# Kernel optimization log

Measured on AMD Instinct MI355X. Metric: run time of the kernel, lower is better.

Reference implementation:

```python
import jax, jax.numpy as jnp
import numpy as np

B, SEQ, D, H, C = 256, 512, 256, 1024, 10
S = SEQ - 1  # module uses seq_length - 1 timesteps


def _kaiming(key, shape):
    fan_in = shape[0]
    return jax.random.normal(key, shape, dtype=jnp.float32) * np.float32(np.sqrt(2.0 / fan_in))


def setup_inputs() -> dict:
    key = jax.random.key(0)
    ks = jax.random.split(key, 12)
    inp = {
        "x": jax.random.randint(ks[0], (B, SEQ), 0, SEQ),
        "emb": jax.random.normal(ks[1], (SEQ, D), dtype=jnp.float32),
        # forward-direction LSTM cell (only modulation g and input i gates affect output
        # because of the source bug: f_out = o_out = sigmoid(i_input))
        "Wgx_f": _kaiming(ks[2], (D, H)), "Wgh_f": _kaiming(ks[3], (H, H)), "bg_f": jnp.zeros((H,), jnp.float32),
        "Wix_f": _kaiming(ks[4], (D, H)), "Wih_f": _kaiming(ks[5], (H, H)), "bi_f": jnp.zeros((H,), jnp.float32),
        # backward-direction LSTM cell
        "Wgx_b": _kaiming(ks[6], (D, H)), "Wgh_b": _kaiming(ks[7], (H, H)), "bg_b": jnp.zeros((H,), jnp.float32),
        "Wix_b": _kaiming(ks[8], (D, H)), "Wih_b": _kaiming(ks[9], (H, H)), "bi_b": jnp.zeros((H,), jnp.float32),
        # prediction head
        "Wp": _kaiming(ks[10], (2 * H, C)), "bp": jnp.zeros((C,), jnp.float32),
    }
    return inp


def _run_lstm(xs, Wgx, Wgh, bg, Wix, Wih, bi):
    # xs: [S, B, D]; returns final hidden state [B, H]
    def step(carry, xt):
        h, c = carry
        g = jnp.tanh(xt @ Wgx + h @ Wgh + bg)
        i = jax.nn.sigmoid(xt @ Wix + h @ Wih + bi)
        # source bug: forget and output gates both equal the input gate i
        c = g * i + i * c
        h = jnp.tanh(c) * i
        return (h, c), None
    h0 = jnp.zeros((xs.shape[1], Wgh.shape[0]), xs.dtype)
    (h, _), _ = jax.lax.scan(step, (h0, h0), xs)
    return h


def reference(x, emb, Wgx_f, Wgh_f, bg_f, Wix_f, Wih_f, bi_f,
              Wgx_b, Wgh_b, bg_b, Wix_b, Wih_b, bi_b, Wp, bp):
    e = emb[x]                              # [B, SEQ, D]
    xs = jnp.transpose(e[:, :S], (1, 0, 2))  # [S, B, D]; last token unused (seq_length-1 steps)
    hf = _run_lstm(xs, Wgx_f, Wgh_f, bg_f, Wix_f, Wih_f, bi_f)
    hb = _run_lstm(xs[::-1], Wgx_b, Wgh_b, bg_b, Wix_b, Wih_b, bi_b)
    Hcat = jnp.concatenate([hf, hb], axis=1)  # [B, 2H]
    return Hcat @ Wp + bp                     # [B, C]
```

## Files before the change

kernel.cpp:

```cpp
#include <hip/hip_runtime.h>
#include <hip/hip_fp16.h>

typedef _Float16 half8 __attribute__((ext_vector_type(8)));
typedef float f32x4 __attribute__((ext_vector_type(4)));
typedef unsigned u32x4 __attribute__((ext_vector_type(4)));
typedef unsigned long long u64;

#define B_ 256
#define SEQ_ 512
#define D_ 256
#define H_ 1024
#define C_ 10
#define S_ 511
#define KB_ 40
#define NPK_ 2048
#define NTF_ 128
#define LP_ 84

#define WPK_HALVES (2*KB_*NTF_*512)
#define EMBH_OFF   (WPK_HALVES*2)
#define EMBH_HALVES (SEQ_*D_)
#define HPK_OFF    (EMBH_OFF + EMBH_HALVES*2)
#define HPK_PER_PAR (2*32*16*64*8)
#define HFIN_OFF   (HPK_OFF + 2*HPK_PER_PAR*2)
#define HFIN_FLOATS (2*B_*H_)
#define BIAS_OFF   (HFIN_OFF + HFIN_FLOATS*4)
#define BAR_OFF    (BIAS_OFF + 2*NPK_*4)
#define BAR_WORDS  (8*32*16)
#define XT_OFF     (BAR_OFF + BAR_WORDS*4)
#define XT_INTS    (SEQ_*B_)
#define XCD_OFF    (XT_OFF + XT_INTS*4)
#define XCD_WORDS  256

__device__ __forceinline__ float fast_sigm(float x) {
    return __builtin_amdgcn_rcpf(1.f + __builtin_amdgcn_exp2f(-1.442695041f * x));
}
__device__ __forceinline__ float fast_tanh(float x) {
    return 1.f - 2.f * __builtin_amdgcn_rcpf(1.f + __builtin_amdgcn_exp2f(2.885390082f * x));
}
__device__ __forceinline__ half8 load_h_uc(const _Float16* p) {
    u64 two[2];
    two[0] = __hip_atomic_load((const u64*)p,     __ATOMIC_RELAXED, __HIP_MEMORY_SCOPE_SYSTEM);
    two[1] = __hip_atomic_load((const u64*)p + 1, __ATOMIC_RELAXED, __HIP_MEMORY_SCOPE_SYSTEM);
    half8 r; __builtin_memcpy(&r, two, 16); return r;
}

__global__ void convert_kernel(
    const int* __restrict__ x, const float* __restrict__ emb,
    const float* __restrict__ Wgx_f, const float* __restrict__ Wgh_f, const float* __restrict__ bg_f,
    const float* __restrict__ Wix_f, const float* __restrict__ Wih_f, const float* __restrict__ bi_f,
    const float* __restrict__ Wgx_b, const float* __restrict__ Wgh_b, const float* __restrict__ bg_b,
    const float* __restrict__ Wix_b, const float* __restrict__ Wih_b, const float* __restrict__ bi_b,
    _Float16* __restrict__ Wpk, _Float16* __restrict__ embh, float* __restrict__ biaspk,
    unsigned* __restrict__ bar, int* __restrict__ xT, unsigned* __restrict__ xcdid)
{
    int idx = blockIdx.x * 256 + threadIdx.x;
    if (idx < WPK_HALVES) {
        int j = idx & 7;
        int L = (idx >> 3) & 63;
        int rest = idx >> 9;
        int ntf = rest & (NTF_ - 1);
        int rest2 = rest >> 7;
        int kb = rest2 % KB_;
        int d  = rest2 / KB_;
        int k = kb*32 + ((L >> 4) << 3) + j;
        int p = (ntf << 4) + (L & 15);
        int gate = (p >> 5) & 1;
        int u = ((p >> 6) << 5) + (p & 31);
        float v;
        if (k < D_) {
            const float* W = d ? (gate ? Wix_b : Wgx_b) : (gate ? Wix_f : Wgx_f);
            v = W[k*H_ + u];
        } else {
            const float* W = d ? (gate ? Wih_b : Wgh_b) : (gate ? Wih_f : Wgh_f);
            v = W[(k - D_)*H_ + u];
        }
        Wpk[idx] = (_Float16)v;
    } else if (idx < WPK_HALVES + EMBH_HALVES) {
        int i2 = idx - WPK_HALVES;
        embh[i2] = (_Float16)emb[i2];
    } else if (idx < WPK_HALVES + EMBH_HALVES + 2*NPK_) {
        int i3 = idx - (WPK_HALVES + EMBH_HALVES);
        int d = i3 >> 11;
        int p = i3 & (NPK_ - 1);
        int gate = (p >> 5) & 1;
        int u = ((p >> 6) << 5) + (p & 31);
        const float* bsrc = d ? (gate ? bi_b : bg_b) : (gate ? bi_f : bg_f);
        biaspk[i3] = bsrc[u];
    } else if (idx < WPK_HALVES + EMBH_HALVES + 2*NPK_ + BAR_WORDS) {
        bar[idx - (WPK_HALVES + EMBH_HALVES + 2*NPK_)] = 0u;
    } else if (idx < WPK_HALVES + EMBH_HALVES + 2*NPK_ + BAR_WORDS + XT_INTS) {
        int i5 = idx - (WPK_HALVES + EMBH_HALVES + 2*NPK_ + BAR_WORDS);
        int t = i5 >> 8;
        int m = i5 & (B_ - 1);
        xT[i5] = x[m*SEQ_ + t];
    } else if (idx < WPK_HALVES + EMBH_HALVES + 2*NPK_ + BAR_WORDS + XT_INTS + XCD_WORDS) {
        xcdid[idx - (WPK_HALVES + EMBH_HALVES + 2*NPK_ + BAR_WORDS + XT_INTS)] = 0u;
    }
}

#define ISSUE_PAIR(buf, pr)                                                                     \
    { _Pragma("unroll")                                                                         \
      for (int j2 = 0; j2 < 2; ++j2) {                                                          \
        _Pragma("unroll")                                                                       \
        for (int mt = 0; mt < 4; ++mt) {                                                        \
            const _Float16* hp = hrd + (size_t)(((8*w + (pr)*2 + j2)*16 + (mtblk*4 + mt))*64 + lane)*8; \
            asm volatile("global_load_dwordx4 %0, %1, off sc0" : "=v"(buf[j2*4+mt]) : "v"(hp)); \
        } } }

#define MFMA_PAIR(buf, pr)                                                                      \
    { _Pragma("unroll")                                                                         \
      for (int j2 = 0; j2 < 2; ++j2)                                                            \
        _Pragma("unroll")                                                                       \
        for (int mt = 0; mt < 4; ++mt)                                                          \
          _Pragma("unroll")                                                                     \
          for (int nt = 0; nt < 4; ++nt)                                                        \
            acc[mt][nt] = __builtin_amdgcn_mfma_f32_16x16x32_f16(buf[j2*4+mt], wfh[(pr)*2+j2][nt], acc[mt][nt], 0, 0, 0); }

__global__ __launch_bounds__(256, 1) void persistent_kernel(
    const int* __restrict__ xT, const _Float16* __restrict__ embh,
    const _Float16* __restrict__ Wpk, const float* __restrict__ biaspk,
    _Float16* __restrict__ hpk, float* __restrict__ hfinal,
    unsigned* __restrict__ bar, unsigned* __restrict__ xcdid)
{
    __shared__ float lds[4][64][LP_];

    int group = blockIdx.x & 7;
    int dir   = group >> 2;
    int mtblk = group & 3;
    int ntb   = blockIdx.x >> 3;
    int w    = threadIdx.x >> 6;
    int lane = threadIdx.x & 63;
    int q    = lane >> 4;
    int c16  = lane & 15;
    int u0   = q * 8;

    unsigned* gflags = bar + group * (32*16);

    unsigned myxcc;
    asm volatile("s_getreg_b32 %0, hwreg(HW_REG_XCC_ID)" : "=s"(myxcc));
    myxcc &= 15u;
    if (threadIdx.x == 0)
        __hip_atomic_store(&xcdid[blockIdx.x], myxcc | 0x100u, __ATOMIC_RELAXED, __HIP_MEMORY_SCOPE_SYSTEM);

    const _Float16* Wd = Wpk + (size_t)dir * (KB_*NTF_*512);

    half8 wfx[2][4], wfh[8][4];
    #pragma unroll
    for (int kx = 0; kx < 2; ++kx) {
        #pragma unroll
        for (int nt = 0; nt < 4; ++nt)
            wfx[kx][nt] = *(const half8*)(Wd + (((size_t)(2*w + kx)*NTF_ + (ntb*4 + nt))*64 + lane)*8);
    }
    #pragma unroll
    for (int i = 0; i < 8; ++i) {
        #pragma unroll
        for (int nt = 0; nt < 4; ++nt)
            wfh[i][nt] = *(const half8*)(Wd + (((size_t)(8 + 8*w + i)*NTF_ + (ntb*4 + nt))*64 + lane)*8);
    }

    float bgr[8], bir[8];
    #pragma unroll
    for (int j = 0; j < 8; ++j) {
        bgr[j] = biaspk[dir*NPK_ + ntb*64 + u0 + j];
        bir[j] = biaspk[dir*NPK_ + ntb*64 + 32 + u0 + j];
    }

    bool fast;
    {
        unsigned idv = myxcc | 0x100u;
        for (;;) {
            if (lane < 32)
                idv = __hip_atomic_load(&xcdid[lane*8 + group], __ATOMIC_RELAXED, __HIP_MEMORY_SCOPE_SYSTEM);
            if (__all(idv >= 0x100u)) break;
            __builtin_amdgcn_s_sleep(1);
        }
        fast = __all(idv == (myxcc | 0x100u));
    }

    float creg[8];
    #pragma unroll
    for (int j = 0; j < 8; ++j) creg[j] = 0.f;

    #pragma unroll 1
    for (int t = 0; t < S_; ++t) {
        const _Float16* hrd = hpk + (size_t)(t & 1) * HPK_PER_PAR + dir*(32*16*64*8);
        _Float16*       hwr = hpk + (size_t)((t & 1) ^ 1) * HPK_PER_PAR + dir*(32*16*64*8);
        int t_eff = dir ? (S_ - 1 - t) : t;

        int xr[4];
        #pragma unroll
        for (int mt = 0; mt < 4; ++mt)
            xr[mt] = xT[t_eff*B_ + mtblk*64 + mt*16 + c16];

        f32x4 acc[4][4];
        #pragma unroll
        for (int a = 0; a < 4; ++a)
            #pragma unroll
            for (int b = 0; b < 4; ++b) {
                acc[a][b][0] = 0.f; acc[a][b][1] = 0.f; acc[a][b][2] = 0.f; acc[a][b][3] = 0.f;
            }

        #pragma unroll
        for (int kx = 0; kx < 2; ++kx) {
            int kb = 2*w + kx;
            half8 a[4];
            #pragma unroll
            for (int mt = 0; mt < 4; ++mt)
                a[mt] = *(const half8*)(embh + xr[mt]*D_ + kb*32 + q*8);
            #pragma unroll
            for (int mt = 0; mt < 4; ++mt) {
                #pragma unroll
                for (int nt = 0; nt < 4; ++nt)
                    acc[mt][nt] = __builtin_amdgcn_mfma_f32_16x16x32_f16(a[mt], wfx[kx][nt], acc[mt][nt], 0, 0, 0);
            }
        }

        if (t > 0) {
            unsigned gen = (unsigned)t;
            if (fast) {
                u32x4 fv = {gen, gen, gen, gen};
                for (;;) {
                    if (lane < 32) {
                        const unsigned* fp = gflags + lane*16;
                        asm volatile("global_load_dwordx4 %0, %1, off sc0\n\ts_waitcnt vmcnt(0)"
                                     : "=v"(fv) : "v"(fp) : "memory");
                    }
                    if (__all(fv[0] >= gen && fv[1] >= gen && fv[2] >= gen && fv[3] >= gen)) break;
                    __builtin_amdgcn_s_sleep(1);
                }
                half8 aE[8], aO[8];
                ISSUE_PAIR(aE, 0);
                ISSUE_PAIR(aO, 1);
                asm volatile("s_waitcnt vmcnt(8)" ::: "memory");
                __builtin_amdgcn_sched_barrier(0);
                MFMA_PAIR(aE, 0);
                ISSUE_PAIR(aE, 2);
                asm volatile("s_waitcnt vmcnt(8)" ::: "memory");
                __builtin_amdgcn_sched_barrier(0);
                MFMA_PAIR(aO, 1);
                ISSUE_PAIR(aO, 3);
                asm volatile("s_waitcnt vmcnt(8)" ::: "memory");
                __builtin_amdgcn_sched_barrier(0);
                MFMA_PAIR(aE, 2);
                asm volatile("s_waitcnt vmcnt(0)" ::: "memory");
                __builtin_amdgcn_sched_barrier(0);
                MFMA_PAIR(aO, 3);
            } else {
                unsigned v = gen;
                for (;;) {
                    if (lane < 32)
                        v = __hip_atomic_load(&gflags[lane*16], __ATOMIC_RELAXED, __HIP_MEMORY_SCOPE_SYSTEM);
                    if (__all(v >= gen)) break;
                    __builtin_amdgcn_s_sleep(1);
                }
                #pragma unroll
                for (int i = 0; i < 8; ++i) {
                    int kb2 = 8*w + i;
                    half8 a[4];
                    #pragma unroll
                    for (int mt = 0; mt < 4; ++mt)
                        a[mt] = load_h_uc(hrd + (size_t)((kb2*16 + (mtblk*4 + mt))*64 + lane)*8);
                    #pragma unroll
                    for (int mt = 0; mt < 4; ++mt) {
                        #pragma unroll
                        for (int nt = 0; nt < 4; ++nt)
                            acc[mt][nt] = __builtin_amdgcn_mfma_f32_16x16x32_f16(a[mt], wfh[i][nt], acc[mt][nt], 0, 0, 0);
                    }
                }
            }
        }

        #pragma unroll
        for (int mt = 0; mt < 4; ++mt) {
            #pragma unroll
            for (int nt = 0; nt < 4; ++nt) {
                #pragma unroll
                for (int r = 0; r < 4; ++r)
                    lds[w][mt*16 + q*4 + r][nt*16 + c16] = acc[mt][nt][r];
            }
        }
        __syncthreads();

        {
            int mloc = w*16 + c16;
            int mg   = mtblk*64 + mloc;
            half8 hv;
            float hf[8];
            #pragma unroll
            for (int j = 0; j < 8; ++j) {
                float zg = lds[0][mloc][u0 + j] + lds[1][mloc][u0 + j]
                         + lds[2][mloc][u0 + j] + lds[3][mloc][u0 + j] + bgr[j];
                float zi = lds[0][mloc][32 + u0 + j] + lds[1][mloc][32 + u0 + j]
                         + lds[2][mloc][32 + u0 + j] + lds[3][mloc][32 + u0 + j] + bir[j];
                float g  = fast_tanh(zg);
                float ii = fast_sigm(zi);
                float cn = ii * (g + creg[j]);
                creg[j] = cn;
                float h = fast_tanh(cn) * ii;
                hv[j] = (_Float16)h;
                hf[j] = h;
            }
            _Float16* base = hwr + ((size_t)((ntb*16 + mtblk*4 + w)*64 + lane) * 8);
            if (fast) {
                asm volatile("global_store_dwordx4 %0, %1, off" :: "v"(base), "v"(hv) : "memory");
            } else {
                u64 two[2];
                __builtin_memcpy(two, &hv, 16);
                __hip_atomic_store((u64*)base,     two[0], __ATOMIC_RELAXED, __HIP_MEMORY_SCOPE_SYSTEM);
                __hip_atomic_store((u64*)base + 1, two[1], __ATOMIC_RELAXED, __HIP_MEMORY_SCOPE_SYSTEM);
            }
            if (t == S_ - 1) {
                #pragma unroll
                for (int j = 0; j < 8; ++j)
                    hfinal[dir*(B_*H_) + mg*H_ + ntb*32 + u0 + j] = hf[j];
            }
        }

        if (t != S_ - 1) {
            if (fast) {
                asm volatile("s_waitcnt vmcnt(0)" ::: "memory");
                if (lane == 0) {
                    unsigned* fp = &gflags[ntb*16 + w];
                    unsigned val = (unsigned)(t + 1);
                    asm volatile("global_store_dword %0, %1, off" :: "v"(fp), "v"(val) : "memory");
                }
                __syncthreads();
            } else {
                __builtin_amdgcn_s_waitcnt(0x0F70);
                __syncthreads();
                if (threadIdx.x == 0)
                    __hip_atomic_store(&gflags[ntb*16], (unsigned)(t + 1), __ATOMIC_RELAXED, __HIP_MEMORY_SCOPE_SYSTEM);
            }
        }
    }
}

__global__ void proj_kernel(const float* __restrict__ hfinal,
                            const float* __restrict__ Wp, const float* __restrict__ bp,
                            float* __restrict__ out)
{
    int b = blockIdx.x;
    int lane = threadIdx.x;
    float s[C_];
    #pragma unroll
    for (int c = 0; c < C_; ++c) s[c] = 0.f;
    for (int j = lane; j < 2*H_; j += 64) {
        float hv = (j < H_) ? hfinal[b*H_ + j] : hfinal[B_*H_ + b*H_ + (j - H_)];
        const float* wr = Wp + j*C_;
        #pragma unroll
        for (int c = 0; c < C_; ++c) s[c] += hv * wr[c];
    }
    #pragma unroll
    for (int off = 32; off > 0; off >>= 1) {
        #pragma unroll
        for (int c = 0; c < C_; ++c) s[c] += __shfl_down(s[c], off);
    }
    if (lane == 0) {
        #pragma unroll
        for (int c = 0; c < C_; ++c) out[b*C_ + c] = s[c] + bp[c];
    }
}

extern "C" void kernel_launch(void* const* d_in, const int* in_sizes, int n_in,
                              void* d_out, int out_size, void* d_ws, size_t ws_size,
                              hipStream_t stream)
{
    const int*   x     = (const int*)d_in[0];
    const float* emb   = (const float*)d_in[1];
    const float* Wgx_f = (const float*)d_in[2];
    const float* Wgh_f = (const float*)d_in[3];
    const float* bg_f  = (const float*)d_in[4];
    const float* Wix_f = (const float*)d_in[5];
    const float* Wih_f = (const float*)d_in[6];
    const float* bi_f  = (const float*)d_in[7];
    const float* Wgx_b = (const float*)d_in[8];
    const float* Wgh_b = (const float*)d_in[9];
    const float* bg_b  = (const float*)d_in[10];
    const float* Wix_b = (const float*)d_in[11];
    const float* Wih_b = (const float*)d_in[12];
    const float* bi_b  = (const float*)d_in[13];
    const float* Wp    = (const float*)d_in[14];
    const float* bp    = (const float*)d_in[15];
    float* out = (float*)d_out;

    char* ws = (char*)d_ws;
    _Float16* Wpk    = (_Float16*)(ws + 0);
    _Float16* embh   = (_Float16*)(ws + EMBH_OFF);
    _Float16* hpk    = (_Float16*)(ws + HPK_OFF);
    float*    hfinal = (float*)(ws + HFIN_OFF);
    float*    biaspk = (float*)(ws + BIAS_OFF);
    unsigned* bar    = (unsigned*)(ws + BAR_OFF);
    int*      xT     = (int*)(ws + XT_OFF);
    unsigned* xcdid  = (unsigned*)(ws + XCD_OFF);

    int total = WPK_HALVES + EMBH_HALVES + 2*NPK_ + BAR_WORDS + XT_INTS + XCD_WORDS;
    convert_kernel<<<(total + 255)/256, 256, 0, stream>>>(
        x, emb, Wgx_f, Wgh_f, bg_f, Wix_f, Wih_f, bi_f,
        Wgx_b, Wgh_b, bg_b, Wix_b, Wih_b, bi_b, Wpk, embh, biaspk, bar, xT, xcdid);

    persistent_kernel<<<256, 256, 0, stream>>>(xT, embh, Wpk, biaspk, hpk, hfinal, bar, xcdid);

    proj_kernel<<<B_, 64, 0, stream>>>(hfinal, Wp, bp, out);
}
```

Measured before the change: 2.547 ms.

## Narrow per-wave flag waits, rotate k-block order per tile, vectorize LDS reduction

In the fast path each wave now polls only the 32 producer flags covering its own k-range (the 8 k-blocks it consumes), instead of all 128 flags through dwordx4 loads. This lets it start as soon as its inputs are ready rather than waiting for the global barrier. The k-block order is rotated by the column tile index (ntb), for both the resident recurrent weights and the h loads, so different blocks read different addresses first and contend less on the same lines. The cross-wave LDS gate reduction now uses 128-bit vector loads with a pairwise add tree. The rotation must stay consistent between weights and activations, and the finer-grained waits change the memory-ordering assumptions.

```diff
diff --git a/kernel.cpp b/kernel.cpp
--- a/kernel.cpp
+++ b/kernel.cpp
@@ -102,9 +102,10 @@
 #define ISSUE_PAIR(buf, pr)                                                                     \
     { _Pragma("unroll")                                                                         \
       for (int j2 = 0; j2 < 2; ++j2) {                                                          \
+        int ir = ((pr)*2 + j2 + ntb) & 7;                                                       \
         _Pragma("unroll")                                                                       \
         for (int mt = 0; mt < 4; ++mt) {                                                        \
-            const _Float16* hp = hrd + (size_t)(((8*w + (pr)*2 + j2)*16 + (mtblk*4 + mt))*64 + lane)*8; \
+            const _Float16* hp = hrd + (size_t)(((8*w + ir)*16 + (mtblk*4 + mt))*64 + lane)*8;  \
             asm volatile("global_load_dwordx4 %0, %1, off sc0" : "=v"(buf[j2*4+mt]) : "v"(hp)); \
         } } }
 
@@ -154,9 +155,10 @@
     }
     #pragma unroll
     for (int i = 0; i < 8; ++i) {
+        int ir = (i + ntb) & 7;
         #pragma unroll
         for (int nt = 0; nt < 4; ++nt)
-            wfh[i][nt] = *(const half8*)(Wd + (((size_t)(8 + 8*w + i)*NTF_ + (ntb*4 + nt))*64 + lane)*8);
+            wfh[i][nt] = *(const half8*)(Wd + (((size_t)(8 + 8*w + ir)*NTF_ + (ntb*4 + nt))*64 + lane)*8);
     }
 
     float bgr[8], bir[8];
@@ -219,14 +221,13 @@
         if (t > 0) {
             unsigned gen = (unsigned)t;
             if (fast) {
-                u32x4 fv = {gen, gen, gen, gen};
+                unsigned v = gen;
+                const unsigned* fp = gflags + (8*w + (lane >> 2))*16 + (lane & 3);
                 for (;;) {
-                    if (lane < 32) {
-                        const unsigned* fp = gflags + lane*16;
-                        asm volatile("global_load_dwordx4 %0, %1, off sc0\n\ts_waitcnt vmcnt(0)"
-                                     : "=v"(fv) : "v"(fp) : "memory");
-                    }
-                    if (__all(fv[0] >= gen && fv[1] >= gen && fv[2] >= gen && fv[3] >= gen)) break;
+                    if (lane < 32)
+                        asm volatile("global_load_dword %0, %1, off sc0\n\ts_waitcnt vmcnt(0)"
+                                     : "=v"(v) : "v"(fp) : "memory");
+                    if (__all(v >= gen)) break;
                     __builtin_amdgcn_s_sleep(1);
                 }
                 half8 aE[8], aO[8];
@@ -256,7 +257,7 @@
                 }
                 #pragma unroll
                 for (int i = 0; i < 8; ++i) {
-                    int kb2 = 8*w + i;
+                    int kb2 = 8*w + ((i + ntb) & 7);
                     half8 a[4];
                     #pragma unroll
                     for (int mt = 0; mt < 4; ++mt)
@@ -285,16 +286,40 @@
         {
             int mloc = w*16 + c16;
             int mg   = mtblk*64 + mloc;
+            f32x4 sg0, sg1, si0, si1;
+            {
+                f32x4 g0a = *(const f32x4*)&lds[0][mloc][u0];
+                f32x4 g0b = *(const f32x4*)&lds[1][mloc][u0];
+                f32x4 g0c = *(const f32x4*)&lds[2][mloc][u0];
+                f32x4 g0d = *(const f32x4*)&lds[3][mloc][u0];
+                sg0 = (g0a + g0b) + (g0c + g0d);
+                f32x4 g1a = *(const f32x4*)&lds[0][mloc][u0 + 4];
+                f32x4 g1b = *(const f32x4*)&lds[1][mloc][u0 + 4];
+                f32x4 g1c = *(const f32x4*)&lds[2][mloc][u0 + 4];
+                f32x4 g1d = *(const f32x4*)&lds[3][mloc][u0 + 4];
+                sg1 = (g1a + g1b) + (g1c + g1d);
+                f32x4 i0a = *(const f32x4*)&lds[0][mloc][32 + u0];
+                f32x4 i0b = *(const f32x4*)&lds[1][mloc][32 + u0];
+                f32x4 i0c = *(const f32x4*)&lds[2][mloc][32 + u0];
+                f32x4 i0d = *(const f32x4*)&lds[3][mloc][32 + u0];
+                si0 = (i0a + i0b) + (i0c + i0d);
+                f32x4 i1a = *(const f32x4*)&lds[0][mloc][36 + u0];
+                f32x4 i1b = *(const f32x4*)&lds[1][mloc][36 + u0];
+                f32x4 i1c = *(const f32x4*)&lds[2][mloc][36 + u0];
+                f32x4 i1d = *(const f32x4*)&lds[3][mloc][36 + u0];
+                si1 = (i1a + i1b) + (i1c + i1d);
+            }
+            float zg[8], zi[8];
+            #pragma unroll
+            for (int j = 0; j < 4; ++j) { zg[j]   = sg0[j] + bgr[j];   zi[j]   = si0[j] + bir[j]; }
+            #pragma unroll
+            for (int j = 0; j < 4; ++j) { zg[4+j] = sg1[j] + bgr[4+j]; zi[4+j] = si1[j] + bir[4+j]; }
             half8 hv;
             float hf[8];
             #pragma unroll
             for (int j = 0; j < 8; ++j) {
-                float zg = lds[0][mloc][u0 + j] + lds[1][mloc][u0 + j]
-                         + lds[2][mloc][u0 + j] + lds[3][mloc][u0 + j] + bgr[j];
-                float zi = lds[0][mloc][32 + u0 + j] + lds[1][mloc][32 + u0 + j]
-                         + lds[2][mloc][32 + u0 + j] + lds[3][mloc][32 + u0 + j] + bir[j];
-                float g  = fast_tanh(zg);
-                float ii = fast_sigm(zi);
+                float g  = fast_tanh(zg[j]);
+                float ii = fast_sigm(zi[j]);
                 float cn = ii * (g + creg[j]);
                 creg[j] = cn;
                 float h = fast_tanh(cn) * ii;
@@ -321,9 +346,9 @@
             if (fast) {
                 asm volatile("s_waitcnt vmcnt(0)" ::: "memory");
                 if (lane == 0) {
-                    unsigned* fp = &gflags[ntb*16 + w];
+                    unsigned* fp2 = &gflags[ntb*16 + w];
                     unsigned val = (unsigned)(t + 1);
-                    asm volatile("global_store_dword %0, %1, off" :: "v"(fp), "v"(val) : "memory");
+                    asm volatile("global_store_dword %0, %1, off" :: "v"(fp2), "v"(val) : "memory");
                 }
                 __syncthreads();
             } else {
```

Result: faster. 2.450 ms (-3.8%).
